# Kernel optimization log

Measured on AMD Instinct MI355X. Metric: run time of the kernel, lower is better.

## Reference

```python
import jax, jax.numpy as jnp
import numpy as np

TOKENS, D_IN, D_OUT = 8192, 4096, 11008


def setup_inputs() -> dict:
    key = jax.random.key(0)
    k1, k2, k3, k4 = jax.random.split(key, 4)
    x = jax.random.normal(k1, (TOKENS, D_IN), dtype=jnp.float32)
    # int8-range quantized weight (stored int32; values in [-127, 127] simulated via [0,127])
    weight_q = jax.random.randint(k2, (D_OUT, D_IN), -127, 128, dtype=jnp.int32)
    # per-output-row scale (abs-max / 127), small positive values
    max_val = jax.random.uniform(k3, (D_OUT,), dtype=jnp.float32, minval=1e-3, maxval=0.02)
    bias = jax.random.normal(k4, (D_OUT,), dtype=jnp.float32)
    return {"x": x, "weight_q": weight_q, "max_val": max_val, "bias": bias}


def reference(x, weight_q, max_val, bias):
    # dequantize: w[o, i] = weight_q[o, i] * max_val[o]   (per-row scale)
    w = weight_q.astype(x.dtype) * max_val[:, None]          # [D_OUT, D_IN]
    # linear: y = x @ w.T + bias
    return jnp.einsum('ti,oi->to', x, w) + bias               # [TOKENS, D_OUT]
```

## Files before the change

kernel.cpp:

```cpp
#include <hip/hip_runtime.h>


#define M_TOK 8192
#define K_DIM 4096
#define N_OUT 11008
#define BM 256
#define BN 256
#define BK 64
#define NT (K_DIM / BK)
#define NBM (M_TOK / BM)
#define NBN (N_OUT / BN)
#define NWG (NBM * NBN)

typedef __attribute__((ext_vector_type(4))) int   i32x4;
typedef __attribute__((ext_vector_type(4))) float f32x4;
typedef __attribute__((ext_vector_type(4))) short bf16x4;
typedef __attribute__((ext_vector_type(8))) short bf16x8;
typedef unsigned short u16;
typedef signed char i8;
typedef unsigned char u8;

__global__ __launch_bounds__(256) void quant_x(const float* __restrict__ x,
                                               i8* __restrict__ xq,
                                               float* __restrict__ sx) {
  const int t = blockIdx.x;
  const int tid = threadIdx.x;
  const float* row = x + (long)t * K_DIM;
  f32x4 v[4];
  float mx = 0.0f;
#pragma unroll
  for (int j = 0; j < 4; ++j) {
    v[j] = ((const f32x4*)row)[tid * 4 + j];
#pragma unroll
    for (int e = 0; e < 4; ++e) mx = fmaxf(mx, fabsf(v[j][e]));
  }
#pragma unroll
  for (int off = 32; off >= 1; off >>= 1) mx = fmaxf(mx, __shfl_xor(mx, off));
  __shared__ float wmx[4];
  if ((tid & 63) == 0) wmx[tid >> 6] = mx;
  __syncthreads();
  mx = fmaxf(fmaxf(wmx[0], wmx[1]), fmaxf(wmx[2], wmx[3]));
  const float sxinv = (mx > 0.0f) ? 127.0f / mx : 0.0f;
  if (tid == 0) sx[t] = (mx > 0.0f) ? mx / 127.0f : 0.0f;
  i32x4 out;
#pragma unroll
  for (int j = 0; j < 4; ++j) {
    int q0 = __float2int_rn(v[j][0] * sxinv);
    int q1 = __float2int_rn(v[j][1] * sxinv);
    int q2 = __float2int_rn(v[j][2] * sxinv);
    int q3 = __float2int_rn(v[j][3] * sxinv);
    q0 = max(-127, min(127, q0)); q1 = max(-127, min(127, q1));
    q2 = max(-127, min(127, q2)); q3 = max(-127, min(127, q3));
    out[j] = (q0 & 255) | ((q1 & 255) << 8) | ((q2 & 255) << 16) | ((q3 & 255) << 24);
  }
  ((i32x4*)(xq + (long)t * K_DIM))[tid] = out;
}

__global__ void pack_w(const int* __restrict__ in, i8* __restrict__ out, long n16) {
  long i = (long)blockIdx.x * blockDim.x + threadIdx.x;
  const long stride = (long)gridDim.x * blockDim.x;
  for (; i < n16; i += stride) {
    i32x4 o;
#pragma unroll
    for (int j = 0; j < 4; ++j) {
      i32x4 w = ((const i32x4*)in)[i * 4 + j];
      o[j] = (w[0] & 255) | ((w[1] & 255) << 8) | ((w[2] & 255) << 16) | ((w[3] & 255) << 24);
    }
    ((i32x4*)out)[i] = o;
  }
}

__device__ __forceinline__ void gl_lds16(const i8* g, u8* l) {
  __builtin_amdgcn_global_load_lds(
      (const __attribute__((address_space(1))) void*)g,
      (__attribute__((address_space(3))) void*)l,
      16, 0, 0);
}

#define STAGE(T) do { \
    u8* wsl = lds + ((T) & 3) * 32768; \
    const int ko = (T) * BK; \
    gl_lds16(pA0 + ko, wsl + dwa); \
    gl_lds16(pA1 + ko, wsl + 8192 + dwa); \
    gl_lds16(pB0 + ko, wsl + 16384 + dwa); \
    gl_lds16(pB1 + ko, wsl + 24576 + dwa); \
  } while (0)

#define TILE_BODY(T, AFC, BVC, AFN, BVN, RA) do { \
    const char* pa_ = ldsc + ((T) & 3) * 32768 + abase; \
    _Pragma("unroll") \
    for (int m = 0; m < 4; ++m) ag[m] = *(const i32x4*)(pa_ + (m + 4) * 1024); \
    if ((T) <= NT - 4) STAGE((T) + 3); \
    __builtin_amdgcn_s_setprio(1); \
    _Pragma("unroll") \
    for (int m = 0; m < 4; ++m) \
      _Pragma("unroll") \
      for (int n = 0; n < 4; ++n) \
        acc[m][n] = __builtin_amdgcn_mfma_i32_16x16x64_i8(AFC[m], BVC[n], acc[m][n], 0, 0, 0); \
    __builtin_amdgcn_s_setprio(0); \
    if (RA) { \
      const char* qa_ = ldsc + (((T) + 1) & 3) * 32768 + abase; \
      const char* qb_ = ldsc + (((T) + 1) & 3) * 32768 + bbase; \
      _Pragma("unroll") \
      for (int m = 0; m < 4; ++m) AFN[m] = *(const i32x4*)(qa_ + m * 1024); \
      _Pragma("unroll") \
      for (int n = 0; n < 4; ++n) BVN[n] = *(const i32x4*)(qb_ + n * 1024); \
    } \
    __builtin_amdgcn_s_setprio(1); \
    _Pragma("unroll") \
    for (int m = 0; m < 4; ++m) \
      _Pragma("unroll") \
      for (int n = 0; n < 4; ++n) \
        acc[m + 4][n] = __builtin_amdgcn_mfma_i32_16x16x64_i8(ag[m], BVC[n], acc[m + 4][n], 0, 0, 0); \
    __builtin_amdgcn_s_setprio(0); \
    if ((T) <= NT - 4) { asm volatile("s_waitcnt vmcnt(4)" ::: "memory"); } \
    else               { asm volatile("s_waitcnt vmcnt(0)" ::: "memory"); } \
    __builtin_amdgcn_sched_barrier(0); \
    __builtin_amdgcn_s_barrier(); \
  } while (0)

__global__ __launch_bounds__(512, 2) void gemm_i8(
    const i8* __restrict__ A, const i8* __restrict__ B,
    const float* __restrict__ sx, const float* __restrict__ scale,
    const float* __restrict__ bias, float* __restrict__ C) {
  __shared__ u8 lds[131072];

  const int tid  = threadIdx.x;
  const int lane = tid & 63;
  const int wave = tid >> 6;
  const int wm = wave >> 2;
  const int wn = wave & 3;

  const int swz = (blockIdx.x & 7) * (NWG / 8) + (blockIdx.x >> 3);
  const int bm = swz / NBN;
  const int bn = swz % NBN;
  const long m0 = (long)bm * BM;
  const long n0 = (long)bn * BN;

  const int rs = tid >> 2;
  const int cs = ((tid & 3) * 16) ^ ((((rs >> 1) & 3)) << 4);
  const i8* pA0 = A + (m0 + rs) * (long)K_DIM + cs;
  const i8* pA1 = pA0 + 128L * K_DIM;
  const i8* pB0 = B + (n0 + rs) * (long)K_DIM + cs;
  const i8* pB1 = pB0 + 128L * K_DIM;
  const int dwa = wave * 1024;

  const int inner = ((lane >> 4) * 16) ^ ((((lane & 15) >> 1) & 3) << 4);
  const int abase = (wm * 128 + (lane & 15)) * 64 + inner;
  const int bbase = 16384 + (wn * 64 + (lane & 15)) * 64 + inner;
  const char* ldsc = (const char*)lds;

  i32x4 acc[8][4] = {};
  i32x4 afE[4], bvE[4], afO[4], bvO[4], ag[4];

  STAGE(0); STAGE(1); STAGE(2);
  asm volatile("s_waitcnt vmcnt(4)" ::: "memory");
  __builtin_amdgcn_sched_barrier(0);
  __builtin_amdgcn_s_barrier();
  {
    const char* qa = ldsc + abase;
    const char* qb = ldsc + bbase;
#pragma unroll
    for (int m = 0; m < 4; ++m) afE[m] = *(const i32x4*)(qa + m * 1024);
#pragma unroll
    for (int n = 0; n < 4; ++n) bvE[n] = *(const i32x4*)(qb + n * 1024);
  }

  for (int t = 0; t < NT - 2; t += 2) {
    TILE_BODY(t,     afE, bvE, afO, bvO, 1);
    TILE_BODY(t + 1, afO, bvO, afE, bvE, 1);
  }
  TILE_BODY(NT - 2, afE, bvE, afO, bvO, 1);
  TILE_BODY(NT - 1, afO, bvO, afE, bvE, 0);

  const int crow = (lane >> 4) * 4;
  const int ccol = lane & 15;
  float sxa[8][4];
#pragma unroll
  for (int m = 0; m < 8; ++m)
#pragma unroll
    for (int v = 0; v < 4; ++v)
      sxa[m][v] = sx[m0 + wm * 128 + m * 16 + crow + v];
#pragma unroll
  for (int n = 0; n < 4; ++n) {
    const long col = n0 + wn * 64 + n * 16 + ccol;
    const float sc = scale[col];
    const float bz = bias[col];
#pragma unroll
    for (int m = 0; m < 8; ++m) {
      const long row = m0 + wm * 128 + m * 16 + crow;
      i32x4 a = acc[m][n];
#pragma unroll
      for (int v = 0; v < 4; ++v)
        C[(row + v) * (long)N_OUT + col] = (float)a[v] * (sc * sxa[m][v]) + bz;
    }
  }
}

__device__ __forceinline__ u16 to_bf16_rne(float f) {
  union { float f; unsigned u; } v; v.f = f;
  return (u16)((v.u + 0x7FFFu + ((v.u >> 16) & 1u)) >> 16);
}

__global__ __launch_bounds__(256) void gemm_cvt(
    const float* __restrict__ X, const int* __restrict__ W,
    const float* __restrict__ scale, const float* __restrict__ bias,
    float* __restrict__ C) {
  __shared__ u16 lds_a[128 * 32];
  __shared__ u16 lds_b[128 * 32];

  const int tid  = threadIdx.x;
  const int lane = tid & 63;
  const int wave = tid >> 6;
  const int wm = wave >> 1, wn = wave & 1;

  const long m0 = (long)blockIdx.y * 128;
  const long n0 = (long)blockIdx.x * 128;

  const int arow = tid >> 3;
  const int acol = (tid & 7) * 4;

  const float* gX = X + (m0 + arow) * (long)K_DIM + acol;
  const int*   gW = W + (n0 + arow) * (long)K_DIM + acol;

  u16* wla = lds_a + arow * 32 + acol;
  u16* wlb = lds_b + arow * 32 + acol;

  f32x4 acc[4][4] = {};
  const int fr = lane & 15;
  const int fk = (lane >> 4) * 8;
  const u16* fa = lds_a + (wm * 64 + fr) * 32 + fk;
  const u16* fb = lds_b + (wn * 64 + fr) * 32 + fk;

  for (int kk = 0; kk < K_DIM / 32; ++kk) {
    const long ko = (long)kk * 32;
    f32x4 xv[4]; i32x4 wv[4];
#pragma unroll
    for (int j = 0; j < 4; ++j) {
      xv[j] = *(const f32x4*)(gX + (long)j * 32 * K_DIM + ko);
      wv[j] = *(const i32x4*)(gW + (long)j * 32 * K_DIM + ko);
    }
    __syncthreads();
#pragma unroll
    for (int j = 0; j < 4; ++j) {
      bf16x4 oa, ob;
      oa.x = (short)to_bf16_rne(xv[j][0]);
      oa.y = (short)to_bf16_rne(xv[j][1]);
      oa.z = (short)to_bf16_rne(xv[j][2]);
      oa.w = (short)to_bf16_rne(xv[j][3]);
      ob.x = (short)to_bf16_rne((float)wv[j][0]);
      ob.y = (short)to_bf16_rne((float)wv[j][1]);
      ob.z = (short)to_bf16_rne((float)wv[j][2]);
      ob.w = (short)to_bf16_rne((float)wv[j][3]);
      *(bf16x4*)(wla + j * 32 * 32) = oa;
      *(bf16x4*)(wlb + j * 32 * 32) = ob;
    }
    __syncthreads();

    bf16x8 af[4], bfr[4];
#pragma unroll
    for (int m = 0; m < 4; ++m) af[m] = *(const bf16x8*)(fa + m * 16 * 32);
#pragma unroll
    for (int n = 0; n < 4; ++n) bfr[n] = *(const bf16x8*)(fb + n * 16 * 32);
#pragma unroll
    for (int m = 0; m < 4; ++m)
#pragma unroll
      for (int n = 0; n < 4; ++n)
        acc[m][n] = __builtin_amdgcn_mfma_f32_16x16x32_bf16(af[m], bfr[n], acc[m][n], 0, 0, 0);
  }

  const int crow = (lane >> 4) * 4;
  const int ccol = lane & 15;
#pragma unroll
  for (int n = 0; n < 4; ++n) {
    const long col = n0 + wn * 64 + n * 16 + ccol;
    const float sc = scale[col];
    const float bz = bias[col];
#pragma unroll
    for (int m = 0; m < 4; ++m) {
      const long row = m0 + wm * 64 + m * 16 + crow;
      f32x4 a = acc[m][n];
#pragma unroll
      for (int v = 0; v < 4; ++v)
        C[(row + v) * (long)N_OUT + col] = a[v] * sc + bz;
    }
  }
}

extern "C" void kernel_launch(void* const* d_in, const int* in_sizes, int n_in,
                              void* d_out, int out_size, void* d_ws, size_t ws_size,
                              hipStream_t stream) {
  const float* x  = (const float*)d_in[0];
  const int*   wq = (const int*)d_in[1];
  const float* mx = (const float*)d_in[2];
  const float* bs = (const float*)d_in[3];
  float* out = (float*)d_out;

  const size_t szXQ = (size_t)M_TOK * K_DIM;
  const size_t szWQ = (size_t)N_OUT * K_DIM;
  const size_t szSX = (size_t)M_TOK * sizeof(float);
  if (ws_size >= szXQ + szWQ + szSX) {
    i8* xq = (i8*)d_ws;
    i8* wq8 = xq + szXQ;
    float* sx = (float*)(wq8 + szWQ);
    quant_x<<<M_TOK, 256, 0, stream>>>(x, xq, sx);
    pack_w<<<2048, 256, 0, stream>>>(wq, wq8, (long)N_OUT * K_DIM / 16);
    gemm_i8<<<dim3(NWG), dim3(512), 0, stream>>>(xq, wq8, sx, mx, bs, out);
  } else {
    dim3 grid(N_OUT / 128, M_TOK / 128);
    gemm_cvt<<<grid, 256, 0, stream>>>(x, wq, mx, bs, out);
  }
}
```

Baseline: 497.1 us.

## Shrink GEMM tile to 128x256 with 4 waves and 3-slot LDS pipeline

Changes the int8 GEMM workgroup from 256x256 with 8 waves to 128x256 with 4 waves. Each wave now covers all 128 rows and 64 columns. The LDS ring goes from four 32KB slots to three 24KB slots, prefetching two tiles ahead instead of three. Fragments are now loaded right before use rather than double-buffered across tiles. The smaller LDS footprint and block size allow more workgroups per CU and double the grid size, but A/B reuse per tile drops and the LDS-read-to-MFMA latency is less hidden.

```diff
diff --git a/kernel.cpp b/kernel.cpp
--- a/kernel.cpp
+++ b/kernel.cpp
@@ -4,13 +4,14 @@
 #define M_TOK 8192
 #define K_DIM 4096
 #define N_OUT 11008
-#define BM 256
+#define BM 128
 #define BN 256
 #define BK 64
 #define NT (K_DIM / BK)
 #define NBM (M_TOK / BM)
 #define NBN (N_OUT / BN)
 #define NWG (NBM * NBN)
+#define SLOT 24576
 
 typedef __attribute__((ext_vector_type(4))) int   i32x4;
 typedef __attribute__((ext_vector_type(4))) float f32x4;
@@ -77,59 +78,55 @@
       16, 0, 0);
 }
 
-#define STAGE(T) do { \
-    u8* wsl = lds + ((T) & 3) * 32768; \
-    const int ko = (T) * BK; \
-    gl_lds16(pA0 + ko, wsl + dwa); \
-    gl_lds16(pA1 + ko, wsl + 8192 + dwa); \
-    gl_lds16(pB0 + ko, wsl + 16384 + dwa); \
-    gl_lds16(pB1 + ko, wsl + 24576 + dwa); \
+#define STAGE(T, WS) do { \
+    u8* wp = lds + (WS); \
+    const int ko_ = (T) * BK; \
+    gl_lds16(pA0 + ko_, wp + dwa); \
+    gl_lds16(pA1 + ko_, wp + 4096 + dwa); \
+    gl_lds16(pB0 + ko_, wp + 8192 + dwa); \
+    gl_lds16(pB1 + ko_, wp + 12288 + dwa); \
+    gl_lds16(pB2 + ko_, wp + 16384 + dwa); \
+    gl_lds16(pB3 + ko_, wp + 20480 + dwa); \
   } while (0)
 
-#define TILE_BODY(T, AFC, BVC, AFN, BVN, RA) do { \
-    const char* pa_ = ldsc + ((T) & 3) * 32768 + abase; \
-    _Pragma("unroll") \
-    for (int m = 0; m < 4; ++m) ag[m] = *(const i32x4*)(pa_ + (m + 4) * 1024); \
-    if ((T) <= NT - 4) STAGE((T) + 3); \
+#define TILE(T, RS, WS, ST, CNTASM) do { \
+    const char* pa_ = ldsc + (RS) + abase; \
+    const char* pb_ = ldsc + (RS) + bbase; \
+    i32x4 af[4], ag4[4], bv[4]; \
+    _Pragma("unroll") \
+    for (int m = 0; m < 4; ++m) af[m] = *(const i32x4*)(pa_ + m * 1024); \
+    _Pragma("unroll") \
+    for (int n = 0; n < 4; ++n) bv[n] = *(const i32x4*)(pb_ + n * 1024); \
+    _Pragma("unroll") \
+    for (int m = 0; m < 4; ++m) ag4[m] = *(const i32x4*)(pa_ + (m + 4) * 1024); \
+    if (ST) STAGE((T) + 2, WS); \
     __builtin_amdgcn_s_setprio(1); \
     _Pragma("unroll") \
     for (int m = 0; m < 4; ++m) \
       _Pragma("unroll") \
       for (int n = 0; n < 4; ++n) \
-        acc[m][n] = __builtin_amdgcn_mfma_i32_16x16x64_i8(AFC[m], BVC[n], acc[m][n], 0, 0, 0); \
-    __builtin_amdgcn_s_setprio(0); \
-    if (RA) { \
-      const char* qa_ = ldsc + (((T) + 1) & 3) * 32768 + abase; \
-      const char* qb_ = ldsc + (((T) + 1) & 3) * 32768 + bbase; \
-      _Pragma("unroll") \
-      for (int m = 0; m < 4; ++m) AFN[m] = *(const i32x4*)(qa_ + m * 1024); \
-      _Pragma("unroll") \
-      for (int n = 0; n < 4; ++n) BVN[n] = *(const i32x4*)(qb_ + n * 1024); \
-    } \
-    __builtin_amdgcn_s_setprio(1); \
+        acc[m][n] = __builtin_amdgcn_mfma_i32_16x16x64_i8(af[m], bv[n], acc[m][n], 0, 0, 0); \
     _Pragma("unroll") \
     for (int m = 0; m < 4; ++m) \
       _Pragma("unroll") \
       for (int n = 0; n < 4; ++n) \
-        acc[m + 4][n] = __builtin_amdgcn_mfma_i32_16x16x64_i8(ag[m], BVC[n], acc[m + 4][n], 0, 0, 0); \
+        acc[m + 4][n] = __builtin_amdgcn_mfma_i32_16x16x64_i8(ag4[m], bv[n], acc[m + 4][n], 0, 0, 0); \
     __builtin_amdgcn_s_setprio(0); \
-    if ((T) <= NT - 4) { asm volatile("s_waitcnt vmcnt(4)" ::: "memory"); } \
-    else               { asm volatile("s_waitcnt vmcnt(0)" ::: "memory"); } \
+    asm volatile(CNTASM ::: "memory"); \
     __builtin_amdgcn_sched_barrier(0); \
     __builtin_amdgcn_s_barrier(); \
   } while (0)
 
-__global__ __launch_bounds__(512, 2) void gemm_i8(
+__global__ __launch_bounds__(256, 2) void gemm_i8(
     const i8* __restrict__ A, const i8* __restrict__ B,
     const float* __restrict__ sx, const float* __restrict__ scale,
     const float* __restrict__ bias, float* __restrict__ C) {
-  __shared__ u8 lds[131072];
+  __shared__ u8 lds[3 * SLOT];
 
   const int tid  = threadIdx.x;
   const int lane = tid & 63;
   const int wave = tid >> 6;
-  const int wm = wave >> 2;
-  const int wn = wave & 3;
+  const int wn   = wave;
 
   const int swz = (blockIdx.x & 7) * (NWG / 8) + (blockIdx.x >> 3);
   const int bm = swz / NBN;
@@ -138,40 +135,38 @@
   const long n0 = (long)bn * BN;
 
   const int rs = tid >> 2;
-  const int cs = ((tid & 3) * 16) ^ ((((rs >> 1) & 3)) << 4);
+  const int cs = ((tid & 3) * 16) ^ (((tid >> 3) & 3) << 4);
   const i8* pA0 = A + (m0 + rs) * (long)K_DIM + cs;
-  const i8* pA1 = pA0 + 128L * K_DIM;
+  const i8* pA1 = pA0 + 64L * K_DIM;
   const i8* pB0 = B + (n0 + rs) * (long)K_DIM + cs;
-  const i8* pB1 = pB0 + 128L * K_DIM;
+  const i8* pB1 = pB0 + 64L * K_DIM;
+  const i8* pB2 = pB0 + 128L * K_DIM;
+  const i8* pB3 = pB0 + 192L * K_DIM;
   const int dwa = wave * 1024;
 
   const int inner = ((lane >> 4) * 16) ^ ((((lane & 15) >> 1) & 3) << 4);
-  const int abase = (wm * 128 + (lane & 15)) * 64 + inner;
-  const int bbase = 16384 + (wn * 64 + (lane & 15)) * 64 + inner;
+  const int abase = (lane & 15) * 64 + inner;
+  const int bbase = 8192 + (wn * 64 + (lane & 15)) * 64 + inner;
   const char* ldsc = (const char*)lds;
 
   i32x4 acc[8][4] = {};
-  i32x4 afE[4], bvE[4], afO[4], bvO[4], ag[4];
-
-  STAGE(0); STAGE(1); STAGE(2);
-  asm volatile("s_waitcnt vmcnt(4)" ::: "memory");
+
+  STAGE(0, 0);
+  STAGE(1, SLOT);
+  asm volatile("s_waitcnt vmcnt(6)" ::: "memory");
   __builtin_amdgcn_sched_barrier(0);
   __builtin_amdgcn_s_barrier();
-  {
-    const char* qa = ldsc + abase;
-    const char* qb = ldsc + bbase;
-#pragma unroll
-    for (int m = 0; m < 4; ++m) afE[m] = *(const i32x4*)(qa + m * 1024);
-#pragma unroll
-    for (int n = 0; n < 4; ++n) bvE[n] = *(const i32x4*)(qb + n * 1024);
-  }
-
-  for (int t = 0; t < NT - 2; t += 2) {
-    TILE_BODY(t,     afE, bvE, afO, bvO, 1);
-    TILE_BODY(t + 1, afO, bvO, afE, bvE, 1);
-  }
-  TILE_BODY(NT - 2, afE, bvE, afO, bvO, 1);
-  TILE_BODY(NT - 1, afO, bvO, afE, bvE, 0);
+
+  int t = 0;
+  for (int tt = 0; tt < (NT - 4) / 3; ++tt) {
+    TILE(t, 0 * SLOT, 2 * SLOT, 1, "s_waitcnt vmcnt(6)"); ++t;
+    TILE(t, 1 * SLOT, 0 * SLOT, 1, "s_waitcnt vmcnt(6)"); ++t;
+    TILE(t, 2 * SLOT, 1 * SLOT, 1, "s_waitcnt vmcnt(6)"); ++t;
+  }
+  TILE(60, 0 * SLOT, 2 * SLOT, 1, "s_waitcnt vmcnt(6)");
+  TILE(61, 1 * SLOT, 0 * SLOT, 1, "s_waitcnt vmcnt(6)");
+  TILE(62, 2 * SLOT, 0,        0, "s_waitcnt vmcnt(0)");
+  TILE(63, 0 * SLOT, 0,        0, "s_waitcnt vmcnt(0)");
 
   const int crow = (lane >> 4) * 4;
   const int ccol = lane & 15;
@@ -180,7 +175,7 @@
   for (int m = 0; m < 8; ++m)
 #pragma unroll
     for (int v = 0; v < 4; ++v)
-      sxa[m][v] = sx[m0 + wm * 128 + m * 16 + crow + v];
+      sxa[m][v] = sx[m0 + m * 16 + crow + v];
 #pragma unroll
   for (int n = 0; n < 4; ++n) {
     const long col = n0 + wn * 64 + n * 16 + ccol;
@@ -188,7 +183,7 @@
     const float bz = bias[col];
 #pragma unroll
     for (int m = 0; m < 8; ++m) {
-      const long row = m0 + wm * 128 + m * 16 + crow;
+      const long row = m0 + m * 16 + crow;
       i32x4 a = acc[m][n];
 #pragma unroll
       for (int v = 0; v < 4; ++v)
@@ -305,7 +300,7 @@
     float* sx = (float*)(wq8 + szWQ);
     quant_x<<<M_TOK, 256, 0, stream>>>(x, xq, sx);
     pack_w<<<2048, 256, 0, stream>>>(wq, wq8, (long)N_OUT * K_DIM / 16);
-    gemm_i8<<<dim3(NWG), dim3(512), 0, stream>>>(xq, wq8, sx, mx, bs, out);
+    gemm_i8<<<dim3(NWG), dim3(256), 0, stream>>>(xq, wq8, sx, mx, bs, out);
   } else {
     dim3 grid(N_OUT / 128, M_TOK / 128);
     gemm_cvt<<<grid, 256, 0, stream>>>(x, wq, mx, bs, out);
```

Result: slower. 585.0 us (+17.7%).
